# Optimization experiments

Measured on AMD Instinct MI355X. Metric: run time of the kernel, lower is better.

The kernel has to match this reference:

```python
import jax, jax.numpy as jnp
import numpy as np

N = 16384        # genes
N_REG = 8192     # regulons (rows of adj)
D_MODEL = 256
OUT_DIM = 128
ALPHA = 0.2      # leaky relu slope
NEG_INF = -9e15  # matches float(-9000000000000000.0)


def setup_inputs() -> dict:
    key = jax.random.key(0)
    k1, k2, k3, k4 = jax.random.split(key, 4)
    inp = jax.random.normal(k1, (N, D_MODEL), dtype=jnp.float32)
    adj = jax.random.randint(k2, (N_REG, N), 0, 2).astype(jnp.float32)
    # xavier_uniform with gain=1.414
    def xavier(k, shape, gain=1.414):
        fan_in, fan_out = shape[0], shape[1]
        a = gain * np.sqrt(6.0 / (fan_in + fan_out))
        return jax.random.uniform(k, shape, jnp.float32, -a, a)
    weights = xavier(k3, (D_MODEL, OUT_DIM))
    a_values = xavier(k4, (2 * OUT_DIM, 1))
    return {"input": inp, "adj_mat": adj, "weights": weights, "a_values": a_values}


def reference(input, adj_mat, weights, a_values):
    out_dim = weights.shape[1]
    n_reg = adj_mat.shape[0]
    w_h = input @ weights                                   # [N, out_dim]
    w_h1 = w_h[:n_reg] @ a_values[:out_dim]                 # [n_reg, 1]
    w_h2 = w_h @ a_values[out_dim:]                         # [N, 1]
    e = jax.nn.leaky_relu(w_h1 + w_h2.T, negative_slope=ALPHA)  # [n_reg, N]
    # masked attention: zero where adj==0, multiply by adj, fill zeros with -9e15
    att = jnp.where(adj_mat != 0, e, jnp.zeros_like(e)) * adj_mat
    att = jnp.where(att == 0, jnp.float32(NEG_INF), att)
    att = jax.nn.softmax(att, axis=1)
    # dropout is identity in eval mode (training=False)
    result = att @ w_h                                      # [n_reg, out_dim]
    return jax.nn.elu(result)                               # concat=True -> ELU
```

## Files before the change

kernel.cpp:

```cpp
#include <hip/hip_runtime.h>
#include <hip/hip_bf16.h>

typedef __bf16 bf16x8 __attribute__((ext_vector_type(8)));
typedef float  f32x4  __attribute__((ext_vector_type(4)));

#define NGENE  16384
#define NREG   8192
#define DMODEL 256
#define ODIM   128
#define KSPLIT 16
#define KCHUNK (NGENE / KSPLIT)
#define NSTEP  (KCHUNK / 32)
#define ALPHA  0.2f

__device__ __forceinline__ float bf2f(unsigned short u) {
  union { unsigned int i; float f; } v; v.i = ((unsigned int)u) << 16; return v.f;
}
__device__ __forceinline__ unsigned short f2bf(float f) {
  __bf16 b = (__bf16)f;
  return __builtin_bit_cast(unsigned short, b);
}
__device__ __forceinline__ void gl_lds16(const void* g, void* l) {
  __builtin_amdgcn_global_load_lds(
      (const __attribute__((address_space(1))) unsigned int*)g,
      (__attribute__((address_space(3))) unsigned int*)l, 16, 0, 0);
}

__global__ void k_detect(const unsigned int* __restrict__ adj_raw,
                         int* __restrict__ flag) {
  if (threadIdx.x == 0 && blockIdx.x == 0) {
    int isbf16 = 0;
    for (int i = 0; i < 256; ++i)
      if ((adj_raw[i] & 0xffffu) == 0x3f80u) isbf16 = 1;
    *flag = isbf16;
  }
}

__global__ void k_wt(const void* __restrict__ W, const void* __restrict__ AVin,
                     const int* __restrict__ flag,
                     unsigned short* __restrict__ WThi,
                     unsigned short* __restrict__ WTlo,
                     float* __restrict__ AVf) {
  const int n = blockIdx.x, k = threadIdx.x;
  const int bf = *flag;
  float w = bf ? bf2f(((const unsigned short*)W)[k * ODIM + n])
               : ((const float*)W)[k * ODIM + n];
  unsigned short h = f2bf(w);
  WThi[n * DMODEL + k] = h;
  WTlo[n * DMODEL + k] = f2bf(w - bf2f(h));
  if (n == 0)
    AVf[k] = bf ? bf2f(((const unsigned short*)AVin)[k]) : ((const float*)AVin)[k];
}

__global__ __launch_bounds__(256) void k_wh(
    const void* __restrict__ X, const int* __restrict__ flag,
    const unsigned short* __restrict__ WThi,
    const unsigned short* __restrict__ WTlo,
    const float* __restrict__ AVf,
    unsigned short* __restrict__ WhThi, unsigned short* __restrict__ WhTlo,
    float* __restrict__ w1, float* __restrict__ w2) {
  __shared__ float lds[4][16][ODIM + 1];
  const int tid = threadIdx.x;
  const int w = tid >> 6, l = tid & 63;
  const int q = l >> 4, ln = l & 15;
  const int m0 = blockIdx.x * 64 + w * 16;

  f32x4 acc[8];
#pragma unroll
  for (int t = 0; t < 8; ++t) acc[t] = (f32x4){0.f, 0.f, 0.f, 0.f};

  const int bf = *flag;
  if (bf) {
    const unsigned short* Xb = (const unsigned short*)X;
#pragma unroll
    for (int ks = 0; ks < 8; ++ks) {
      const int k0 = ks * 32 + q * 8;
      bf16x8 a = *(const bf16x8*)(Xb + (size_t)(m0 + ln) * DMODEL + k0);
#pragma unroll
      for (int t = 0; t < 8; ++t) {
        bf16x8 bh = *(const bf16x8*)(WThi + (size_t)(16 * t + ln) * DMODEL + k0);
        bf16x8 bl = *(const bf16x8*)(WTlo + (size_t)(16 * t + ln) * DMODEL + k0);
        acc[t] = __builtin_amdgcn_mfma_f32_16x16x32_bf16(a, bh, acc[t], 0, 0, 0);
        acc[t] = __builtin_amdgcn_mfma_f32_16x16x32_bf16(a, bl, acc[t], 0, 0, 0);
      }
    }
  } else {
    const float* Xf = (const float*)X;
#pragma unroll
    for (int ks = 0; ks < 8; ++ks) {
      const int k0 = ks * 32 + q * 8;
      const float* xp = Xf + (size_t)(m0 + ln) * DMODEL + k0;
      f32x4 x0 = *(const f32x4*)xp, x1 = *(const f32x4*)(xp + 4);
      bf16x8 ah, al;
#pragma unroll
      for (int j = 0; j < 8; ++j) {
        float xv = (j < 4) ? x0[j] : x1[j - 4];
        __bf16 hb = (__bf16)xv;
        ah[j] = hb;
        al[j] = (__bf16)(xv - (float)hb);
      }
#pragma unroll
      for (int t = 0; t < 8; ++t) {
        bf16x8 bh = *(const bf16x8*)(WThi + (size_t)(16 * t + ln) * DMODEL + k0);
        bf16x8 bl = *(const bf16x8*)(WTlo + (size_t)(16 * t + ln) * DMODEL + k0);
        acc[t] = __builtin_amdgcn_mfma_f32_16x16x32_bf16(ah, bh, acc[t], 0, 0, 0);
        acc[t] = __builtin_amdgcn_mfma_f32_16x16x32_bf16(ah, bl, acc[t], 0, 0, 0);
        acc[t] = __builtin_amdgcn_mfma_f32_16x16x32_bf16(al, bh, acc[t], 0, 0, 0);
      }
    }
  }

  float a1v[8], a2v[8];
#pragma unroll
  for (int t = 0; t < 8; ++t) {
    a1v[t] = AVf[16 * t + ln];
    a2v[t] = AVf[ODIM + 16 * t + ln];
  }
#pragma unroll
  for (int r = 0; r < 4; ++r) {
    float s1 = 0.f, s2 = 0.f;
#pragma unroll
    for (int t = 0; t < 8; ++t) {
      s1 += acc[t][r] * a1v[t];
      s2 += acc[t][r] * a2v[t];
    }
    s1 += __shfl_xor(s1, 1); s1 += __shfl_xor(s1, 2);
    s1 += __shfl_xor(s1, 4); s1 += __shfl_xor(s1, 8);
    s2 += __shfl_xor(s2, 1); s2 += __shfl_xor(s2, 2);
    s2 += __shfl_xor(s2, 4); s2 += __shfl_xor(s2, 8);
    const int row = m0 + q * 4 + r;
    if (ln == 0) {
      w2[row] = s2;
      if (row < NREG) w1[row] = s1;
    }
  }

#pragma unroll
  for (int t = 0; t < 8; ++t)
#pragma unroll
    for (int r = 0; r < 4; ++r)
      lds[w][q * 4 + r][16 * t + ln] = acc[t][r];
  __syncthreads();

#pragma unroll
  for (int rr = 0; rr < 2; ++rr) {
    const int n = 2 * l + rr;
    unsigned short oh[16], ol[16];
#pragma unroll
    for (int m = 0; m < 16; ++m) {
      float v = lds[w][m][n];
      unsigned short h = f2bf(v);
      oh[m] = h;
      ol[m] = f2bf(v - bf2f(h));
    }
    uint4* dh = (uint4*)(WhThi + (size_t)n * NGENE + m0);
    dh[0] = ((uint4*)oh)[0]; dh[1] = ((uint4*)oh)[1];
    uint4* dl = (uint4*)(WhTlo + (size_t)n * NGENE + m0);
    dl[0] = ((uint4*)ol)[0]; dl[1] = ((uint4*)ol)[1];
  }
}

__device__ __forceinline__ void att_compute(
    const float* av0, const float* av1, const float* w2v,
    const unsigned char* lsh, const unsigned char* lsl,
    int q, int ln, float w1v0, float w1v1,
    f32x4* acc0, f32x4* acc1, float& ssum0, float& ssum1) {
  bf16x8 af0, af1;
#pragma unroll
  for (int j = 0; j < 8; ++j) {
    float s0 = w1v0 + w2v[j];
    float p0 = av0[j] * __expf(fmaxf(s0, ALPHA * s0));
    __bf16 pb0 = (__bf16)p0;
    af0[j] = pb0; ssum0 += (float)pb0;
    float s1 = w1v1 + w2v[j];
    float p1 = av1[j] * __expf(fmaxf(s1, ALPHA * s1));
    __bf16 pb1 = (__bf16)p1;
    af1[j] = pb1; ssum1 += (float)pb1;
  }
#pragma unroll
  for (int t = 0; t < 8; ++t) {
    int n = 16 * t + ln;
    int s = n * 4 + (q ^ ((n >> 1) & 3));
    bf16x8 bh = *(const bf16x8*)(lsh + s * 16);
    bf16x8 bl = *(const bf16x8*)(lsl + s * 16);
    acc0[t] = __builtin_amdgcn_mfma_f32_16x16x32_bf16(af0, bh, acc0[t], 0, 0, 0);
    acc0[t] = __builtin_amdgcn_mfma_f32_16x16x32_bf16(af0, bl, acc0[t], 0, 0, 0);
    acc1[t] = __builtin_amdgcn_mfma_f32_16x16x32_bf16(af1, bh, acc1[t], 0, 0, 0);
    acc1[t] = __builtin_amdgcn_mfma_f32_16x16x32_bf16(af1, bl, acc1[t], 0, 0, 0);
  }
}

__global__ __launch_bounds__(128) void k_att(
    const void* __restrict__ adj, const int* __restrict__ flag,
    const unsigned short* __restrict__ WhThi,
    const unsigned short* __restrict__ WhTlo,
    const float* __restrict__ w1, const float* __restrict__ w2,
    float* __restrict__ Opart, float* __restrict__ Spart) {
  __shared__ __align__(16) unsigned char ls[2][8192];
  const int tid = threadIdx.x;
  const int w = tid >> 6, l = tid & 63;
  const int q = l >> 4, ln = l & 15;
  const int mb = blockIdx.x & 127;
  const int kc = blockIdx.x >> 7;
  const int m0 = mb * 64 + w * 32;
  const int r0 = m0 + ln, r1 = m0 + 16 + ln;
  const int kbase = kc * KCHUNK;

  const float w1v0 = w1[r0], w1v1 = w1[r1];

  size_t soff[4];
  int ldsoff[4];
#pragma unroll
  for (int i = 0; i < 4; ++i) {
    int s = i * 128 + tid;
    int n = s >> 2;
    int qs = (s & 3) ^ ((n >> 1) & 3);
    soff[i] = (size_t)n * NGENE + qs * 8;
    ldsoff[i] = (i * 128 + w * 64) * 16;
  }
  auto stage = [&](int kglob) {
#pragma unroll
    for (int i = 0; i < 4; ++i) {
      gl_lds16(WhThi + soff[i] + kglob, &ls[0][ldsoff[i]]);
      gl_lds16(WhTlo + soff[i] + kglob, &ls[1][ldsoff[i]]);
    }
  };

  f32x4 acc0[8], acc1[8];
#pragma unroll
  for (int t = 0; t < 8; ++t) {
    acc0[t] = (f32x4){0.f, 0.f, 0.f, 0.f};
    acc1[t] = (f32x4){0.f, 0.f, 0.f, 0.f};
  }
  float ssum0 = 0.f, ssum1 = 0.f;
  const float* wp = w2 + kbase + q * 8;

  if (*flag) {
    const unsigned short* A = (const unsigned short*)adj;
    const unsigned short* ap0 = A + (size_t)r0 * NGENE + kbase + q * 8;
    const unsigned short* ap1 = A + (size_t)r1 * NGENE + kbase + q * 8;
    uint4 c0 = *(const uint4*)ap0;
    uint4 c1 = *(const uint4*)ap1;
    f32x4 wa = *(const f32x4*)wp, wb = *(const f32x4*)(wp + 4);
    stage(kbase);
    for (int st = 0; st < NSTEP; ++st) {
      __syncthreads();
      uint4 u0 = c0, u1 = c1; f32x4 va = wa, vb = wb;
      if (st + 1 < NSTEP) {
        c0 = *(const uint4*)(ap0 + (st + 1) * 32);
        c1 = *(const uint4*)(ap1 + (st + 1) * 32);
        wa = *(const f32x4*)(wp + (st + 1) * 32);
        wb = *(const f32x4*)(wp + (st + 1) * 32 + 4);
      }
      float av0[8], av1[8], w2v[8];
      const unsigned int* p0w = (const unsigned int*)&u0;
      const unsigned int* p1w = (const unsigned int*)&u1;
#pragma unroll
      for (int j = 0; j < 8; ++j) {
        union { unsigned int i; float f; } x, y;
        x.i = (j & 1) ? (p0w[j >> 1] & 0xffff0000u) : (p0w[j >> 1] << 16);
        y.i = (j & 1) ? (p1w[j >> 1] & 0xffff0000u) : (p1w[j >> 1] << 16);
        av0[j] = x.f; av1[j] = y.f;
        w2v[j] = (j < 4) ? va[j] : vb[j - 4];
      }
      att_compute(av0, av1, w2v, ls[0], ls[1], q, ln, w1v0, w1v1,
                  acc0, acc1, ssum0, ssum1);
      __syncthreads();
      if (st + 1 < NSTEP) stage(kbase + (st + 1) * 32);
    }
  } else {
    const float* A = (const float*)adj;
    const float* ap0 = A + (size_t)r0 * NGENE + kbase + q * 8;
    const float* ap1 = A + (size_t)r1 * NGENE + kbase + q * 8;
    f32x4 c0a = *(const f32x4*)ap0,       c0b = *(const f32x4*)(ap0 + 4);
    f32x4 c1a = *(const f32x4*)ap1,       c1b = *(const f32x4*)(ap1 + 4);
    f32x4 wa = *(const f32x4*)wp, wb = *(const f32x4*)(wp + 4);
    stage(kbase);
    for (int st = 0; st < NSTEP; ++st) {
      __syncthreads();
      f32x4 u0a = c0a, u0b = c0b, u1a = c1a, u1b = c1b;
      f32x4 va = wa, vb = wb;
      if (st + 1 < NSTEP) {
        c0a = *(const f32x4*)(ap0 + (st + 1) * 32);
        c0b = *(const f32x4*)(ap0 + (st + 1) * 32 + 4);
        c1a = *(const f32x4*)(ap1 + (st + 1) * 32);
        c1b = *(const f32x4*)(ap1 + (st + 1) * 32 + 4);
        wa = *(const f32x4*)(wp + (st + 1) * 32);
        wb = *(const f32x4*)(wp + (st + 1) * 32 + 4);
      }
      float av0[8], av1[8], w2v[8];
#pragma unroll
      for (int j = 0; j < 8; ++j) {
        av0[j] = (j < 4) ? u0a[j] : u0b[j - 4];
        av1[j] = (j < 4) ? u1a[j] : u1b[j - 4];
        w2v[j] = (j < 4) ? va[j] : vb[j - 4];
      }
      att_compute(av0, av1, w2v, ls[0], ls[1], q, ln, w1v0, w1v1,
                  acc0, acc1, ssum0, ssum1);
      __syncthreads();
      if (st + 1 < NSTEP) stage(kbase + (st + 1) * 32);
    }
  }

  ssum0 += __shfl_xor(ssum0, 16); ssum0 += __shfl_xor(ssum0, 32);
  ssum1 += __shfl_xor(ssum1, 16); ssum1 += __shfl_xor(ssum1, 32);
  if (l < 16) {
    Spart[(size_t)kc * NREG + r0] = ssum0;
    Spart[(size_t)kc * NREG + r1] = ssum1;
  }
  float* op0 = Opart + ((size_t)kc * NREG + m0) * ODIM;
  float* op1 = op0 + 16 * ODIM;
#pragma unroll
  for (int t = 0; t < 8; ++t)
#pragma unroll
    for (int r = 0; r < 4; ++r) {
      op0[(q * 4 + r) * ODIM + 16 * t + ln] = acc0[t][r];
      op1[(q * 4 + r) * ODIM + 16 * t + ln] = acc1[t][r];
    }
}

__global__ void k_red(const float* __restrict__ Opart,
                      const float* __restrict__ Spart,
                      const int* __restrict__ flag, void* __restrict__ out) {
  const int id = blockIdx.x * 256 + threadIdx.x;
  const int row = id >> 7;
  float o = 0.f, s = 0.f;
#pragma unroll
  for (int k = 0; k < KSPLIT; ++k) {
    o += Opart[(size_t)k * (NREG * ODIM) + id];
    s += Spart[(size_t)k * NREG + row];
  }
  const float r = o / s;
  const float res = r > 0.f ? r : (__expf(r) - 1.f);
  if (*flag) ((unsigned short*)out)[id] = f2bf(res);
  else       ((float*)out)[id] = res;
}

extern "C" void kernel_launch(void* const* d_in, const int* in_sizes, int n_in,
                              void* d_out, int out_size, void* d_ws, size_t ws_size,
                              hipStream_t stream) {
  const void* X   = d_in[0];
  const void* ADJ = d_in[1];
  const void* W   = d_in[2];
  const void* AV  = d_in[3];

  char* ws = (char*)d_ws;
  size_t off = 0;
  auto alloc = [&](size_t bytes) -> void* {
    void* p = ws + off; off += (bytes + 255) & ~(size_t)255; return p;
  };
  unsigned short* WhThi = (unsigned short*)alloc((size_t)ODIM * NGENE * 2);
  unsigned short* WhTlo = (unsigned short*)alloc((size_t)ODIM * NGENE * 2);
  unsigned short* WThi  = (unsigned short*)alloc((size_t)DMODEL * ODIM * 2);
  unsigned short* WTlo  = (unsigned short*)alloc((size_t)DMODEL * ODIM * 2);
  float* AVf   = (float*)alloc(2 * ODIM * 4);
  float* w1    = (float*)alloc((size_t)NREG * 4);
  float* w2    = (float*)alloc((size_t)NGENE * 4);
  int*   flag  = (int*)alloc(256);
  float* Spart = (float*)alloc((size_t)KSPLIT * NREG * 4);
  float* Opart = (float*)alloc((size_t)KSPLIT * NREG * ODIM * 4);

  hipLaunchKernelGGL(k_detect, dim3(1), dim3(64), 0, stream,
                     (const unsigned int*)ADJ, flag);
  hipLaunchKernelGGL(k_wt, dim3(ODIM), dim3(DMODEL), 0, stream,
                     W, AV, flag, WThi, WTlo, AVf);
  hipLaunchKernelGGL(k_wh, dim3(NGENE / 64), dim3(256), 0, stream,
                     X, flag, WThi, WTlo, AVf, WhThi, WhTlo, w1, w2);
  hipLaunchKernelGGL(k_att, dim3(128 * KSPLIT), dim3(128), 0, stream,
                     ADJ, flag, WhThi, WhTlo, w1, w2, Opart, Spart);
  hipLaunchKernelGGL(k_red, dim3((NREG * ODIM) / 256), dim3(256), 0, stream,
                     Opart, Spart, flag, d_out);
}
```

Measured before the change: 867.8 us.

## Drop hi/lo bf16 split, double-buffer LDS staging, enlarge attention blocks

Removes the hi/lo bf16 split of W and Wh, so each GEMM uses one bf16 operand, halving MFMA work and staging traffic in the attention kernel and cutting it to a third in the Wh projection on the fp32 path. Adds a double-buffered LDS ring so the next tile's global-to-LDS load overlaps compute, which drops one barrier per step. Attention blocks grow to 256 threads covering 128 rows, and KSPLIT drops from 16 to 8, shrinking the partial-sum buffers and reduction work. The trade-off is lower precision in Wh and the attention weights, which risks accuracy tolerance.

```diff
diff --git a/kernel.cpp b/kernel.cpp
--- a/kernel.cpp
+++ b/kernel.cpp
@@ -8,7 +8,7 @@
 #define NREG   8192
 #define DMODEL 256
 #define ODIM   128
-#define KSPLIT 16
+#define KSPLIT 8
 #define KCHUNK (NGENE / KSPLIT)
 #define NSTEP  (KCHUNK / 32)
 #define ALPHA  0.2f
@@ -38,26 +38,21 @@
 
 __global__ void k_wt(const void* __restrict__ W, const void* __restrict__ AVin,
                      const int* __restrict__ flag,
-                     unsigned short* __restrict__ WThi,
-                     unsigned short* __restrict__ WTlo,
+                     unsigned short* __restrict__ WT,
                      float* __restrict__ AVf) {
   const int n = blockIdx.x, k = threadIdx.x;
   const int bf = *flag;
   float w = bf ? bf2f(((const unsigned short*)W)[k * ODIM + n])
                : ((const float*)W)[k * ODIM + n];
-  unsigned short h = f2bf(w);
-  WThi[n * DMODEL + k] = h;
-  WTlo[n * DMODEL + k] = f2bf(w - bf2f(h));
+  WT[n * DMODEL + k] = f2bf(w);
   if (n == 0)
     AVf[k] = bf ? bf2f(((const unsigned short*)AVin)[k]) : ((const float*)AVin)[k];
 }
 
 __global__ __launch_bounds__(256) void k_wh(
     const void* __restrict__ X, const int* __restrict__ flag,
-    const unsigned short* __restrict__ WThi,
-    const unsigned short* __restrict__ WTlo,
-    const float* __restrict__ AVf,
-    unsigned short* __restrict__ WhThi, unsigned short* __restrict__ WhTlo,
+    const unsigned short* __restrict__ WT, const float* __restrict__ AVf,
+    unsigned short* __restrict__ WhT,
     float* __restrict__ w1, float* __restrict__ w2) {
   __shared__ float lds[4][16][ODIM + 1];
   const int tid = threadIdx.x;
@@ -70,43 +65,22 @@
   for (int t = 0; t < 8; ++t) acc[t] = (f32x4){0.f, 0.f, 0.f, 0.f};
 
   const int bf = *flag;
-  if (bf) {
-    const unsigned short* Xb = (const unsigned short*)X;
-#pragma unroll
-    for (int ks = 0; ks < 8; ++ks) {
-      const int k0 = ks * 32 + q * 8;
-      bf16x8 a = *(const bf16x8*)(Xb + (size_t)(m0 + ln) * DMODEL + k0);
-#pragma unroll
-      for (int t = 0; t < 8; ++t) {
-        bf16x8 bh = *(const bf16x8*)(WThi + (size_t)(16 * t + ln) * DMODEL + k0);
-        bf16x8 bl = *(const bf16x8*)(WTlo + (size_t)(16 * t + ln) * DMODEL + k0);
-        acc[t] = __builtin_amdgcn_mfma_f32_16x16x32_bf16(a, bh, acc[t], 0, 0, 0);
-        acc[t] = __builtin_amdgcn_mfma_f32_16x16x32_bf16(a, bl, acc[t], 0, 0, 0);
-      }
-    }
-  } else {
-    const float* Xf = (const float*)X;
-#pragma unroll
-    for (int ks = 0; ks < 8; ++ks) {
-      const int k0 = ks * 32 + q * 8;
-      const float* xp = Xf + (size_t)(m0 + ln) * DMODEL + k0;
+#pragma unroll
+  for (int ks = 0; ks < 8; ++ks) {
+    const int k0 = ks * 32 + q * 8;
+    bf16x8 a;
+    if (bf) {
+      a = *(const bf16x8*)((const unsigned short*)X + (size_t)(m0 + ln) * DMODEL + k0);
+    } else {
+      const float* xp = (const float*)X + (size_t)(m0 + ln) * DMODEL + k0;
       f32x4 x0 = *(const f32x4*)xp, x1 = *(const f32x4*)(xp + 4);
-      bf16x8 ah, al;
-#pragma unroll
-      for (int j = 0; j < 8; ++j) {
-        float xv = (j < 4) ? x0[j] : x1[j - 4];
-        __bf16 hb = (__bf16)xv;
-        ah[j] = hb;
-        al[j] = (__bf16)(xv - (float)hb);
-      }
-#pragma unroll
-      for (int t = 0; t < 8; ++t) {
-        bf16x8 bh = *(const bf16x8*)(WThi + (size_t)(16 * t + ln) * DMODEL + k0);
-        bf16x8 bl = *(const bf16x8*)(WTlo + (size_t)(16 * t + ln) * DMODEL + k0);
-        acc[t] = __builtin_amdgcn_mfma_f32_16x16x32_bf16(ah, bh, acc[t], 0, 0, 0);
-        acc[t] = __builtin_amdgcn_mfma_f32_16x16x32_bf16(ah, bl, acc[t], 0, 0, 0);
-        acc[t] = __builtin_amdgcn_mfma_f32_16x16x32_bf16(al, bh, acc[t], 0, 0, 0);
-      }
+#pragma unroll
+      for (int j = 0; j < 8; ++j) a[j] = (__bf16)((j < 4) ? x0[j] : x1[j - 4]);
+    }
+#pragma unroll
+    for (int t = 0; t < 8; ++t) {
+      bf16x8 b = *(const bf16x8*)(WT + (size_t)(16 * t + ln) * DMODEL + k0);
+      acc[t] = __builtin_amdgcn_mfma_f32_16x16x32_bf16(a, b, acc[t], 0, 0, 0);
     }
   }
 
@@ -145,25 +119,17 @@
 #pragma unroll
   for (int rr = 0; rr < 2; ++rr) {
     const int n = 2 * l + rr;
-    unsigned short oh[16], ol[16];
-#pragma unroll
-    for (int m = 0; m < 16; ++m) {
-      float v = lds[w][m][n];
-      unsigned short h = f2bf(v);
-      oh[m] = h;
-      ol[m] = f2bf(v - bf2f(h));
-    }
-    uint4* dh = (uint4*)(WhThi + (size_t)n * NGENE + m0);
+    unsigned short oh[16];
+#pragma unroll
+    for (int m = 0; m < 16; ++m) oh[m] = f2bf(lds[w][m][n]);
+    uint4* dh = (uint4*)(WhT + (size_t)n * NGENE + m0);
     dh[0] = ((uint4*)oh)[0]; dh[1] = ((uint4*)oh)[1];
-    uint4* dl = (uint4*)(WhTlo + (size_t)n * NGENE + m0);
-    dl[0] = ((uint4*)ol)[0]; dl[1] = ((uint4*)ol)[1];
   }
 }
 
 __device__ __forceinline__ void att_compute(
     const float* av0, const float* av1, const float* w2v,
-    const unsigned char* lsh, const unsigned char* lsl,
-    int q, int ln, float w1v0, float w1v1,
+    const unsigned char* lsb, int q, int ln, float w1v0, float w1v1,
     f32x4* acc0, f32x4* acc1, float& ssum0, float& ssum1) {
   bf16x8 af0, af1;
 #pragma unroll
@@ -181,49 +147,43 @@
   for (int t = 0; t < 8; ++t) {
     int n = 16 * t + ln;
     int s = n * 4 + (q ^ ((n >> 1) & 3));
-    bf16x8 bh = *(const bf16x8*)(lsh + s * 16);
-    bf16x8 bl = *(const bf16x8*)(lsl + s * 16);
-    acc0[t] = __builtin_amdgcn_mfma_f32_16x16x32_bf16(af0, bh, acc0[t], 0, 0, 0);
-    acc0[t] = __builtin_amdgcn_mfma_f32_16x16x32_bf16(af0, bl, acc0[t], 0, 0, 0);
-    acc1[t] = __builtin_amdgcn_mfma_f32_16x16x32_bf16(af1, bh, acc1[t], 0, 0, 0);
-    acc1[t] = __builtin_amdgcn_mfma_f32_16x16x32_bf16(af1, bl, acc1[t], 0, 0, 0);
-  }
-}
-
-__global__ __launch_bounds__(128) void k_att(
+    bf16x8 b = *(const bf16x8*)(lsb + s * 16);
+    acc0[t] = __builtin_amdgcn_mfma_f32_16x16x32_bf16(af0, b, acc0[t], 0, 0, 0);
+    acc1[t] = __builtin_amdgcn_mfma_f32_16x16x32_bf16(af1, b, acc1[t], 0, 0, 0);
+  }
+}
+
+__global__ __launch_bounds__(256) void k_att(
     const void* __restrict__ adj, const int* __restrict__ flag,
-    const unsigned short* __restrict__ WhThi,
-    const unsigned short* __restrict__ WhTlo,
+    const unsigned short* __restrict__ WhT,
     const float* __restrict__ w1, const float* __restrict__ w2,
     float* __restrict__ Opart, float* __restrict__ Spart) {
   __shared__ __align__(16) unsigned char ls[2][8192];
   const int tid = threadIdx.x;
   const int w = tid >> 6, l = tid & 63;
   const int q = l >> 4, ln = l & 15;
-  const int mb = blockIdx.x & 127;
-  const int kc = blockIdx.x >> 7;
-  const int m0 = mb * 64 + w * 32;
+  const int mb = blockIdx.x & 63;
+  const int kc = blockIdx.x >> 6;
+  const int m0 = mb * 128 + w * 32;
   const int r0 = m0 + ln, r1 = m0 + 16 + ln;
   const int kbase = kc * KCHUNK;
 
   const float w1v0 = w1[r0], w1v1 = w1[r1];
 
-  size_t soff[4];
-  int ldsoff[4];
-#pragma unroll
-  for (int i = 0; i < 4; ++i) {
-    int s = i * 128 + tid;
+  size_t soff[2];
+  int ldsoff[2];
+#pragma unroll
+  for (int i = 0; i < 2; ++i) {
+    int s = i * 256 + tid;
     int n = s >> 2;
     int qs = (s & 3) ^ ((n >> 1) & 3);
     soff[i] = (size_t)n * NGENE + qs * 8;
-    ldsoff[i] = (i * 128 + w * 64) * 16;
-  }
-  auto stage = [&](int kglob) {
-#pragma unroll
-    for (int i = 0; i < 4; ++i) {
-      gl_lds16(WhThi + soff[i] + kglob, &ls[0][ldsoff[i]]);
-      gl_lds16(WhTlo + soff[i] + kglob, &ls[1][ldsoff[i]]);
-    }
+    ldsoff[i] = (i * 256 + w * 64) * 16;
+  }
+  auto stage = [&](int kglob, int buf) {
+#pragma unroll
+    for (int i = 0; i < 2; ++i)
+      gl_lds16(WhT + soff[i] + kglob, &ls[buf][ldsoff[i]]);
   };
 
   f32x4 acc0[8], acc1[8];
@@ -234,6 +194,8 @@
   }
   float ssum0 = 0.f, ssum1 = 0.f;
   const float* wp = w2 + kbase + q * 8;
+
+  stage(kbase, 0);
 
   if (*flag) {
     const unsigned short* A = (const unsigned short*)adj;
@@ -242,9 +204,9 @@
     uint4 c0 = *(const uint4*)ap0;
     uint4 c1 = *(const uint4*)ap1;
     f32x4 wa = *(const f32x4*)wp, wb = *(const f32x4*)(wp + 4);
-    stage(kbase);
     for (int st = 0; st < NSTEP; ++st) {
       __syncthreads();
+      if (st + 1 < NSTEP) stage(kbase + (st + 1) * 32, (st + 1) & 1);
       uint4 u0 = c0, u1 = c1; f32x4 va = wa, vb = wb;
       if (st + 1 < NSTEP) {
         c0 = *(const uint4*)(ap0 + (st + 1) * 32);
@@ -263,21 +225,19 @@
         av0[j] = x.f; av1[j] = y.f;
         w2v[j] = (j < 4) ? va[j] : vb[j - 4];
       }
-      att_compute(av0, av1, w2v, ls[0], ls[1], q, ln, w1v0, w1v1,
+      att_compute(av0, av1, w2v, ls[st & 1], q, ln, w1v0, w1v1,
                   acc0, acc1, ssum0, ssum1);
-      __syncthreads();
-      if (st + 1 < NSTEP) stage(kbase + (st + 1) * 32);
     }
   } else {
     const float* A = (const float*)adj;
     const float* ap0 = A + (size_t)r0 * NGENE + kbase + q * 8;
     const float* ap1 = A + (size_t)r1 * NGENE + kbase + q * 8;
-    f32x4 c0a = *(const f32x4*)ap0,       c0b = *(const f32x4*)(ap0 + 4);
-    f32x4 c1a = *(const f32x4*)ap1,       c1b = *(const f32x4*)(ap1 + 4);
+    f32x4 c0a = *(const f32x4*)ap0, c0b = *(const f32x4*)(ap0 + 4);
+    f32x4 c1a = *(const f32x4*)ap1, c1b = *(const f32x4*)(ap1 + 4);
     f32x4 wa = *(const f32x4*)wp, wb = *(const f32x4*)(wp + 4);
-    stage(kbase);
     for (int st = 0; st < NSTEP; ++st) {
       __syncthreads();
+      if (st + 1 < NSTEP) stage(kbase + (st + 1) * 32, (st + 1) & 1);
       f32x4 u0a = c0a, u0b = c0b, u1a = c1a, u1b = c1b;
       f32x4 va = wa, vb = wb;
       if (st + 1 < NSTEP) {
@@ -295,10 +255,8 @@
         av1[j] = (j < 4) ? u1a[j] : u1b[j - 4];
         w2v[j] = (j < 4) ? va[j] : vb[j - 4];
       }
-      att_compute(av0, av1, w2v, ls[0], ls[1], q, ln, w1v0, w1v1,
+      att_compute(av0, av1, w2v, ls[st & 1], q, ln, w1v0, w1v1,
                   acc0, acc1, ssum0, ssum1);
-      __syncthreads();
-      if (st + 1 < NSTEP) stage(kbase + (st + 1) * 32);
     }
   }
 
@@ -349,10 +307,8 @@
   auto alloc = [&](size_t bytes) -> void* {
     void* p = ws + off; off += (bytes + 255) & ~(size_t)255; return p;
   };
-  unsigned short* WhThi = (unsigned short*)alloc((size_t)ODIM * NGENE * 2);
-  unsigned short* WhTlo = (unsigned short*)alloc((size_t)ODIM * NGENE * 2);
-  unsigned short* WThi  = (unsigned short*)alloc((size_t)DMODEL * ODIM * 2);
-  unsigned short* WTlo  = (unsigned short*)alloc((size_t)DMODEL * ODIM * 2);
+  unsigned short* WhT = (unsigned short*)alloc((size_t)ODIM * NGENE * 2);
+  unsigned short* WT  = (unsigned short*)alloc((size_t)DMODEL * ODIM * 2);
   float* AVf   = (float*)alloc(2 * ODIM * 4);
   float* w1    = (float*)alloc((size_t)NREG * 4);
   float* w2    = (float*)alloc((size_t)NGENE * 4);
@@ -363,11 +319,11 @@
   hipLaunchKernelGGL(k_detect, dim3(1), dim3(64), 0, stream,
                      (const unsigned int*)ADJ, flag);
   hipLaunchKernelGGL(k_wt, dim3(ODIM), dim3(DMODEL), 0, stream,
-                     W, AV, flag, WThi, WTlo, AVf);
+                     W, AV, flag, WT, AVf);
   hipLaunchKernelGGL(k_wh, dim3(NGENE / 64), dim3(256), 0, stream,
-                     X, flag, WThi, WTlo, AVf, WhThi, WhTlo, w1, w2);
-  hipLaunchKernelGGL(k_att, dim3(128 * KSPLIT), dim3(128), 0, stream,
-                     ADJ, flag, WhThi, WhTlo, w1, w2, Opart, Spart);
+                     X, flag, WT, AVf, WhT, w1, w2);
+  hipLaunchKernelGGL(k_att, dim3(64 * KSPLIT), dim3(256), 0, stream,
+                     ADJ, flag, WhT, w1, w2, Opart, Spart);
   hipLaunchKernelGGL(k_red, dim3((NREG * ODIM) / 256), dim3(256), 0, stream,
                      Opart, Spart, flag, d_out);
 }
```

Result: faster. 760.0 us (-12.4%).
